# Performance work log

Hardware: AMD Instinct MI355X
Metric: run time of the kernel (lower is better)

The kernel has to match this reference:

```python
import jax, jax.numpy as jnp
import numpy as np

GROUP = 128

def _dequant(q, s, z):
    # q: [O, K] int4 values in [0,16); s,z: [O, K//GROUP]
    O, K = q.shape
    qg = q.reshape(O, K // GROUP, GROUP)
    w = (qg - z[:, :, None]).astype(s.dtype) * s[:, :, None]
    return w.reshape(O, K)

def setup_inputs() -> dict:
    key = jax.random.key(0)
    ks = jax.random.split(key, 7)
    H, I = 4096, 14336
    x = jax.random.normal(ks[0], (2, 2048, H), jnp.float32)
    q_up = jax.random.randint(ks[1], (I, H), 0, 16, jnp.int32)
    s_up = (jax.random.uniform(ks[2], (I, H // GROUP), jnp.float32) * 0.02 + 1e-3)
    z_up = jax.random.randint(ks[3], (I, H // GROUP), 0, 16, jnp.int32)
    q_down = jax.random.randint(ks[4], (H, I), 0, 16, jnp.int32)
    s_down = (jax.random.uniform(ks[5], (H, I // GROUP), jnp.float32) * 0.02 + 1e-3)
    z_down = jax.random.randint(ks[6], (H, I // GROUP), 0, 16, jnp.int32)
    return {"x": x, "q_up": q_up, "s_up": s_up, "z_up": z_up,
            "q_down": q_down, "s_down": s_down, "z_down": z_down}

def reference(x, q_up, s_up, z_up, q_down, s_down, z_down):
    # up_proj: W4A16 dequant + GEMM, weight layout [out, in] like nn.Linear
    w_up = _dequant(q_up, s_up, z_up)        # [I, H]
    h = jnp.einsum('bsh,ih->bsi', x, w_up)   # [B, S, I]
    # NemotronH 'relu2' activation: relu(h)^2
    a = jnp.square(jax.nn.relu(h))
    w_down = _dequant(q_down, s_down, z_down)  # [H, I]
    y = jnp.einsum('bsi,hi->bsh', a, w_down)   # [B, S, H]
    return y
```

## Files before the change

kernel.cpp:

```cpp
#include <hip/hip_runtime.h>
#include <stdint.h>

typedef unsigned short u16;
typedef __attribute__((ext_vector_type(4))) float f32x4;
typedef __attribute__((ext_vector_type(8))) __bf16 bf16x8;
typedef __attribute__((ext_vector_type(8))) unsigned short u16x8;

__device__ __forceinline__ u16 f2bf(float f) {
  unsigned u = __builtin_bit_cast(unsigned, f);
  u = (u + 0x7fffu + ((u >> 16) & 1u)) >> 16;
  return (u16)u;
}

typedef __attribute__((address_space(1))) const void gvoid_t;
typedef __attribute__((address_space(3))) void lvoid_t;

__device__ __forceinline__ void gload_lds16(const void* g, void* l) {
  __builtin_amdgcn_global_load_lds((gvoid_t*)g, (lvoid_t*)l, 16, 0, 0);
}

__global__ __launch_bounds__(256)
void dequant_kernel(const int* __restrict__ q, const float* __restrict__ s,
                    const int* __restrict__ z, u16* __restrict__ w, int K) {
  const int row = blockIdx.y;
  const int k = (blockIdx.x * 256 + threadIdx.x) << 3;
  const int ng = K >> 7;
  const int g = k >> 7;
  const float sv = s[(size_t)row * ng + g];
  const float zv = (float)z[(size_t)row * ng + g];
  const int4* qp = (const int4*)(q + (size_t)row * K + k);
  const int4 a = qp[0], b = qp[1];
  u16x8 o;
  o[0] = f2bf(((float)a.x - zv) * sv);
  o[1] = f2bf(((float)a.y - zv) * sv);
  o[2] = f2bf(((float)a.z - zv) * sv);
  o[3] = f2bf(((float)a.w - zv) * sv);
  o[4] = f2bf(((float)b.x - zv) * sv);
  o[5] = f2bf(((float)b.y - zv) * sv);
  o[6] = f2bf(((float)b.z - zv) * sv);
  o[7] = f2bf(((float)b.w - zv) * sv);
  *reinterpret_cast<u16x8*>(w + (size_t)row * K + k) = o;
}

__global__ __launch_bounds__(256)
void cvt_kernel(const float* __restrict__ in, u16* __restrict__ out) {
  const size_t i = ((size_t)blockIdx.x * 256 + threadIdx.x) << 3;
  const float4* p = (const float4*)(in + i);
  const float4 a = p[0], b = p[1];
  u16x8 o;
  o[0] = f2bf(a.x); o[1] = f2bf(a.y); o[2] = f2bf(a.z); o[3] = f2bf(a.w);
  o[4] = f2bf(b.x); o[5] = f2bf(b.y); o[6] = f2bf(b.z); o[7] = f2bf(b.w);
  *reinterpret_cast<u16x8*>(out + i) = o;
}

template<bool RELU2>
__global__ __launch_bounds__(512, 2)
void gemm256(const u16* __restrict__ Ap, const u16* __restrict__ Bp,
             void* __restrict__ Cptr, int M, int N, int K) {
  __shared__ __align__(16) u16 As[2][256][64];
  __shared__ __align__(16) u16 Bs[2][256][64];
  const int tid = threadIdx.x;
  const int lane = tid & 63;
  const int wid = tid >> 6;
  const int wr = wid >> 2, wc = wid & 3;

  const int nbx = N >> 8;
  const int nwg = gridDim.x;
  int bid = blockIdx.x;
  bid = (bid & 7) * (nwg >> 3) + (bid >> 3);
  const int m0 = (bid / nbx) << 8;
  const int n0 = (bid % nbx) << 8;

  const int srow = tid >> 3;
  const int scol = tid & 7;
  const int lr = lane & 15;
  const int lk = (lane >> 4) << 3;
  const int xorc = (lr & 7) << 3;

  const char* baA0 = (const char*)&As[0][0][0] + (wr * 128 + lr) * 128;
  const char* baA1 = baA0 + 32768;
  const char* baB0 = (const char*)&Bs[0][0][0] + (wc * 64 + lr) * 128;
  const char* baB1 = baB0 + 32768;
  const int koff0 = (lk ^ xorc) * 2;

  f32x4 acc[8][4] = {};
  bf16x8 a1[4], a2[4], a3[4], a4[4], b1[4], b2[4];

  const int nk = K >> 6;

#define STG_A(bufi, h, kt) do { _Pragma("unroll") \
  for (int l_ = 0; l_ < 2; ++l_) { \
    const int r_ = (h) * 128 + l_ * 64 + srow; \
    gload_lds16(Ap + (size_t)(m0 + r_) * K + (size_t)((kt) << 6) + ((scol ^ (srow & 7)) << 3), \
                &As[bufi][r_][scol << 3]); } } while (0)
#define STG_B(bufi, h, kt) do { _Pragma("unroll") \
  for (int l_ = 0; l_ < 2; ++l_) { \
    const int r_ = (h) * 128 + l_ * 64 + srow; \
    gload_lds16(Bp + (size_t)(n0 + r_) * K + (size_t)((kt) << 6) + ((scol ^ (srow & 7)) << 3), \
                &Bs[bufi][r_][scol << 3]); } } while (0)
#define RD_A(base, ks, half, dst) do { _Pragma("unroll") \
  for (int i_ = 0; i_ < 4; ++i_) \
    dst[i_] = *reinterpret_cast<const bf16x8*>( \
      (base) + ((half) * 4 + i_) * 2048 + (koff0 ^ ((ks) * 64))); } while (0)
#define RD_B(base, ks, dst) do { _Pragma("unroll") \
  for (int j_ = 0; j_ < 4; ++j_) \
    dst[j_] = *reinterpret_cast<const bf16x8*>( \
      (base) + j_ * 2048 + (koff0 ^ ((ks) * 64))); } while (0)
#define MFMA16(ASET, BSET, I0) do { _Pragma("unroll") \
  for (int i_ = 0; i_ < 4; ++i_) { _Pragma("unroll") \
    for (int j_ = 0; j_ < 4; ++j_) \
      acc[(I0) + i_][j_] = __builtin_amdgcn_mfma_f32_16x16x32_bf16( \
        ASET[i_], BSET[j_], acc[(I0) + i_][j_], 0, 0, 0); } } while (0)
#define BARO() do { asm volatile("" ::: "memory"); __builtin_amdgcn_s_barrier(); \
  asm volatile("" ::: "memory"); } while (0)
#define LGKM(n) do { asm volatile("s_waitcnt lgkmcnt(" #n ")" ::: "memory"); \
  __builtin_amdgcn_sched_barrier(0); } while (0)
#define SB0 __builtin_amdgcn_sched_barrier(0)
#define GATE4 asm volatile("s_waitcnt vmcnt(4)" ::: "memory")
#define PRIO(Q) do { __builtin_amdgcn_s_setprio(1); Q; __builtin_amdgcn_s_setprio(0); } while (0)
#define TILE4(bA, bB, SA1, SA2, SB3, SB4) do { \
  BARO(); \
  RD_B(bB, 0, b1); RD_A(bA, 0, 0, a1); \
  LGKM(0); \
  SA1; \
  PRIO(MFMA16(a1, b1, 0)); \
  SB0; RD_B(bB, 1, b2); SB0; RD_A(bA, 0, 1, a2); SB0; RD_A(bA, 1, 1, a4); SB0; RD_A(bA, 1, 0, a3); \
  BARO(); \
  LGKM(8); \
  SA2; \
  PRIO(MFMA16(a2, b1, 4)); \
  BARO(); \
  LGKM(4); \
  SB3; \
  PRIO(MFMA16(a4, b2, 4)); \
  BARO(); \
  LGKM(0); \
  SB4; \
  PRIO(MFMA16(a3, b2, 0)); \
  GATE4; \
} while (0)

  STG_A(0, 0, 0); STG_A(0, 1, 0);
  STG_B(0, 0, 0); STG_B(0, 1, 0);
  STG_B(1, 0, 1); STG_B(1, 1, 1);
  asm volatile("s_waitcnt vmcnt(4)" ::: "memory");

  const int nit = nk >> 1;
  for (int it = 0; it < nit; ++it) {
    const int t1 = 2 * it + 1;
    int t2 = 2 * it + 2; if (t2 >= nk) t2 -= nk;
    int t3 = 2 * it + 3; if (t3 >= nk) t3 -= nk;
    TILE4(baA0, baB0, STG_A(1, 0, t1), STG_A(1, 1, t1), STG_B(0, 0, t2), STG_B(0, 1, t2));
    TILE4(baA1, baB1, STG_A(0, 0, t2), STG_A(0, 1, t2), STG_B(1, 0, t3), STG_B(1, 1, t3));
  }
  asm volatile("s_waitcnt vmcnt(0) lgkmcnt(0)" ::: "memory");

  const int crow = (lane >> 4) << 2;
  const int ccol = lane & 15;
#pragma unroll
  for (int i = 0; i < 8; ++i) {
#pragma unroll
    for (int j = 0; j < 4; ++j) {
#pragma unroll
      for (int q = 0; q < 4; ++q) {
        const int m = m0 + wr * 128 + i * 16 + crow + q;
        const int n = n0 + wc * 64 + j * 16 + ccol;
        const float v = acc[i][j][q];
        if constexpr (RELU2) {
          const float r = fmaxf(v, 0.f);
          ((u16*)Cptr)[(size_t)m * N + n] = f2bf(r * r);
        } else {
          ((float*)Cptr)[(size_t)m * N + n] = v;
        }
      }
    }
  }
#undef STG_A
#undef STG_B
#undef RD_A
#undef RD_B
#undef MFMA16
#undef BARO
#undef LGKM
#undef SB0
#undef GATE4
#undef PRIO
#undef TILE4
}

extern "C" void kernel_launch(void* const* d_in, const int* in_sizes, int n_in,
                              void* d_out, int out_size, void* d_ws, size_t ws_size,
                              hipStream_t stream) {
  const float* x    = (const float*)d_in[0];
  const int*   q_up = (const int*)d_in[1];
  const float* s_up = (const float*)d_in[2];
  const int*   z_up = (const int*)d_in[3];
  const int*   q_dn = (const int*)d_in[4];
  const float* s_dn = (const float*)d_in[5];
  const int*   z_dn = (const int*)d_in[6];
  float* y = (float*)d_out;

  const int H = 4096, I = 14336;
  const int M = in_sizes[0] / H;

  const size_t wbytes = (size_t)I * H * 2;
  const size_t abytes = (size_t)M * I * 2;
  const size_t xbytes = (size_t)M * H * 2;
  u16* wbuf = (u16*)d_ws;
  u16* abuf = (u16*)((char*)d_ws + wbytes);
  u16* xbf  = (u16*)((char*)d_ws + wbytes + abytes);
  if (ws_size < wbytes + abytes + xbytes) return;

  dequant_kernel<<<dim3(H / 8 / 256, I), 256, 0, stream>>>(q_up, s_up, z_up, wbuf, H);
  cvt_kernel<<<dim3((int)(((size_t)M * H) >> 11)), 256, 0, stream>>>(x, xbf);
  gemm256<true><<<dim3((M / 256) * (I / 256)), 512, 0, stream>>>(xbf, wbuf, abuf, M, I, H);
  dequant_kernel<<<dim3(I / 8 / 256, H), 256, 0, stream>>>(q_dn, s_dn, z_dn, wbuf, I);
  gemm256<false><<<dim3((M / 256) * (H / 256)), 512, 0, stream>>>(abuf, wbuf, y, M, H, I);
}
```

Before: 952.5 us.

## Fold down-proj weight dequant into up-proj GEMM grid as extra blocks

Appends H/2 extra workgroups to the up-projection GEMM launch. Each one dequantizes two rows of the down-projection weight into a separate workspace buffer, so that work overlaps with the GEMM tail instead of running as its own kernel between the GEMMs. This needs a second weight-sized workspace region and falls back to the old path when the workspace is too small. The extra blocks use the GEMM's 512-thread, large-LDS configuration, which may limit how many run at once.

New measurement: 927.7 us. 1.03x faster.

```diff
diff --git a/kernel.cpp b/kernel.cpp
--- a/kernel.cpp
+++ b/kernel.cpp
@@ -56,16 +56,47 @@
 template<bool RELU2>
 __global__ __launch_bounds__(512, 2)
 void gemm256(const u16* __restrict__ Ap, const u16* __restrict__ Bp,
-             void* __restrict__ Cptr, int M, int N, int K) {
+             void* __restrict__ Cptr, int M, int N, int K, int gemmNwg,
+             const int* __restrict__ q2, const float* __restrict__ s2,
+             const int* __restrict__ z2, u16* __restrict__ w2) {
   __shared__ __align__(16) u16 As[2][256][64];
   __shared__ __align__(16) u16 Bs[2][256][64];
+
+  if ((int)blockIdx.x >= gemmNwg) {
+    const int b = (int)blockIdx.x - gemmNwg;
+    const int I2 = 14336, ng = I2 >> 7;
+#pragma unroll
+    for (int itc = 0; itc < 7; ++itc) {
+      const int inner = itc * 4096 + (int)threadIdx.x * 8;
+      const int r = (inner >= I2) ? 1 : 0;
+      const int k = inner - r * I2;
+      const int row = 2 * b + r;
+      const int g = k >> 7;
+      const float sv = s2[(size_t)row * ng + g];
+      const float zv = (float)z2[(size_t)row * ng + g];
+      const int4* qp = (const int4*)(q2 + (size_t)row * I2 + k);
+      const int4 qa = qp[0], qb = qp[1];
+      u16x8 o;
+      o[0] = f2bf(((float)qa.x - zv) * sv);
+      o[1] = f2bf(((float)qa.y - zv) * sv);
+      o[2] = f2bf(((float)qa.z - zv) * sv);
+      o[3] = f2bf(((float)qa.w - zv) * sv);
+      o[4] = f2bf(((float)qb.x - zv) * sv);
+      o[5] = f2bf(((float)qb.y - zv) * sv);
+      o[6] = f2bf(((float)qb.z - zv) * sv);
+      o[7] = f2bf(((float)qb.w - zv) * sv);
+      *reinterpret_cast<u16x8*>(w2 + (size_t)row * I2 + k) = o;
+    }
+    return;
+  }
+
   const int tid = threadIdx.x;
   const int lane = tid & 63;
   const int wid = tid >> 6;
   const int wr = wid >> 2, wc = wid & 3;
 
   const int nbx = N >> 8;
-  const int nwg = gridDim.x;
+  const int nwg = gemmNwg;
   int bid = blockIdx.x;
   bid = (bid & 7) * (nwg >> 3) + (bid >> 3);
   const int m0 = (bid / nbx) << 8;
@@ -206,14 +237,28 @@
   const size_t wbytes = (size_t)I * H * 2;
   const size_t abytes = (size_t)M * I * 2;
   const size_t xbytes = (size_t)M * H * 2;
-  u16* wbuf = (u16*)d_ws;
-  u16* abuf = (u16*)((char*)d_ws + wbytes);
-  u16* xbf  = (u16*)((char*)d_ws + wbytes + abytes);
+  u16* wbuf  = (u16*)d_ws;
+  u16* abuf  = (u16*)((char*)d_ws + wbytes);
+  u16* xbf   = (u16*)((char*)d_ws + wbytes + abytes);
+  u16* wbuf2 = (u16*)((char*)d_ws + wbytes + abytes + xbytes);
   if (ws_size < wbytes + abytes + xbytes) return;
+  const bool fused = ws_size >= 2 * wbytes + abytes + xbytes;
 
   dequant_kernel<<<dim3(H / 8 / 256, I), 256, 0, stream>>>(q_up, s_up, z_up, wbuf, H);
   cvt_kernel<<<dim3((int)(((size_t)M * H) >> 11)), 256, 0, stream>>>(x, xbf);
-  gemm256<true><<<dim3((M / 256) * (I / 256)), 512, 0, stream>>>(xbf, wbuf, abuf, M, I, H);
-  dequant_kernel<<<dim3(I / 8 / 256, H), 256, 0, stream>>>(q_dn, s_dn, z_dn, wbuf, I);
-  gemm256<false><<<dim3((M / 256) * (H / 256)), 512, 0, stream>>>(abuf, wbuf, y, M, H, I);
-}
+
+  const int g1 = (M / 256) * (I / 256);
+  const int g2 = (M / 256) * (H / 256);
+  if (fused) {
+    gemm256<true><<<dim3(g1 + H / 2), 512, 0, stream>>>(
+        xbf, wbuf, abuf, M, I, H, g1, q_dn, s_dn, z_dn, wbuf2);
+    gemm256<false><<<dim3(g2), 512, 0, stream>>>(
+        abuf, wbuf2, y, M, H, I, g2, nullptr, nullptr, nullptr, nullptr);
+  } else {
+    gemm256<true><<<dim3(g1), 512, 0, stream>>>(
+        xbf, wbuf, abuf, M, I, H, g1, nullptr, nullptr, nullptr, nullptr);
+    dequant_kernel<<<dim3(I / 8 / 256, H), 256, 0, stream>>>(q_dn, s_dn, z_dn, wbuf, I);
+    gemm256<false><<<dim3(g2), 512, 0, stream>>>(
+        abuf, wbuf, y, M, H, I, g2, nullptr, nullptr, nullptr, nullptr);
+  }
+}
```
